# Kernel tuning notes

Hardware: AMD Instinct MI355X
Metric: run time of the kernel (lower is better)

Reference implementation:

```python
import jax, jax.numpy as jnp
from jax import lax
import numpy as np

DIVISOR = 2.0

def setup_inputs() -> dict:
    key = jax.random.key(0)
    k1, k2, k3, k4 = jax.random.split(key, 4)
    B, Cin, D, H, W = 64, 8, 32, 64, 64
    Cout, KD, KH, KW = 16, 3, 3, 3
    fan_in = Cin * KD * KH * KW
    bound = 1.0 / np.sqrt(fan_in)
    x = jax.random.normal(k1, (B, Cin, D, H, W), dtype=jnp.float32)
    conv_weight = jax.random.uniform(k2, (Cout, Cin, KD, KH, KW), jnp.float32, -bound, bound)
    conv_bias = jax.random.uniform(k3, (Cout,), jnp.float32, -bound, bound)
    bias = jax.random.normal(k4, (Cout, 1, 1, 1), dtype=jnp.float32) * 0.02
    return {"x": x, "conv_weight": conv_weight, "conv_bias": conv_bias, "bias": bias}

def reference(x, conv_weight, conv_bias, bias):
    # Conv3d, stride 1, no padding, groups=1  -> [B, Cout, D-2, H-2, W-2]
    y = lax.conv_general_dilated(
        x, conv_weight, window_strides=(1, 1, 1), padding='VALID',
        dimension_numbers=('NCDHW', 'OIDHW', 'NCDHW'))
    y = y + conv_bias[None, :, None, None, None]
    # Divide by constant
    y = y / DIVISOR
    # MaxPool3d(kernel=2, stride=2), floor mode (VALID drops the trailing odd row)
    y = lax.reduce_window(y, -jnp.inf, lax.max,
                          window_dimensions=(1, 1, 2, 2, 2),
                          window_strides=(1, 1, 2, 2, 2), padding='VALID')
    # AdaptiveAvgPool3d((1,1,1)) == global mean over spatial dims
    y = jnp.mean(y, axis=(2, 3, 4), keepdims=True)  # [B, Cout, 1, 1, 1]
    # Bias add (broadcast over batch)
    y = y + bias[None]
    # Sum over channel dim (sum_dim=1, no keepdim)
    return jnp.sum(y, axis=1)  # [B, 1, 1, 1]
```

## Files before the change

### kernel.cpp

```cpp
#include <hip/hip_runtime.h>

typedef __attribute__((ext_vector_type(8))) short short8;
typedef __attribute__((ext_vector_type(4))) float f32x4;
typedef unsigned int u32;

#define ROW_B 1056
#define SLOT_B 10560
#define NSLOT 4
#define CSTRIDE 131072

__device__ __forceinline__ unsigned short f2bf(float f) {
  unsigned u = __builtin_bit_cast(unsigned, f);
  u += 0x7FFFu + ((u >> 16) & 1u);
  return (unsigned short)(u >> 16);
}
__device__ __forceinline__ u32 cvtpk(float lo, float hi) {
  u32 r;
  asm("v_cvt_pk_bf16_f32 %0, %1, %2" : "=v"(r) : "v"(lo), "v"(hi));
  return r;
}

#define LBAR()                                                                \
  {                                                                           \
    asm volatile("s_waitcnt lgkmcnt(0)" ::: "memory");                        \
    __builtin_amdgcn_s_barrier();                                             \
    __builtin_amdgcn_sched_barrier(0);                                        \
  }

#define MFMA1(A, B, C) __builtin_amdgcn_mfma_f32_16x16x32_bf16(A, B, C, 0, 0, 0)

#define RDF(SB, WT, R) (*(const short8*)(smem + (SB) + (R) * ROW_B + physoff[WT]))

#define MGRP(F0, F1, F2, F3, WT, AN, AM, AO, K0, K1, K2)                      \
  {                                                                           \
    if (K0) {                                                                 \
      AN[0][WT] = MFMA1(F0, bfragB[0][0], zf4);                               \
      AN[1][WT] = MFMA1(F1, bfragB[0][0], zf4);                               \
      AN[0][WT] = MFMA1(F1, bfragB[0][1], AN[0][WT]);                         \
      AN[1][WT] = MFMA1(F2, bfragB[0][1], AN[1][WT]);                         \
      AN[0][WT] = MFMA1(F2, bfragB[0][2], AN[0][WT]);                         \
      AN[1][WT] = MFMA1(F3, bfragB[0][2], AN[1][WT]);                         \
    }                                                                         \
    if (K1) {                                                                 \
      AM[0][WT] = MFMA1(F0, bfragB[1][0], AM[0][WT]);                         \
      AM[1][WT] = MFMA1(F1, bfragB[1][0], AM[1][WT]);                         \
      AM[0][WT] = MFMA1(F1, bfragB[1][1], AM[0][WT]);                         \
      AM[1][WT] = MFMA1(F2, bfragB[1][1], AM[1][WT]);                         \
      AM[0][WT] = MFMA1(F2, bfragB[1][2], AM[0][WT]);                         \
      AM[1][WT] = MFMA1(F3, bfragB[1][2], AM[1][WT]);                         \
    }                                                                         \
    if (K2) {                                                                 \
      AO[0][WT] = MFMA1(F0, bfragB[2][0], AO[0][WT]);                         \
      AO[1][WT] = MFMA1(F1, bfragB[2][0], AO[1][WT]);                         \
      AO[0][WT] = MFMA1(F1, bfragB[2][1], AO[0][WT]);                         \
      AO[1][WT] = MFMA1(F2, bfragB[2][1], AO[1][WT]);                         \
      AO[0][WT] = MFMA1(F2, bfragB[2][2], AO[0][WT]);                         \
      AO[1][WT] = MFMA1(F3, bfragB[2][2], AO[1][WT]);                         \
    }                                                                         \
  }

#define PROC(DP, AN, AM, AO, PFC, PFN, K0, K1, K2, CL, SV, WR, LD, PF, BAR)   \
  {                                                                           \
    const int dp_  = (DP);                                                    \
    const int sb_  = (dp_ & 3) * SLOT_B + rowbase;                            \
    const int sbn_ = ((dp_ + 1) & 3) * SLOT_B + rowbase;                      \
    short8 t1_0 = RDF(sb_, 1, 0), t1_1 = RDF(sb_, 1, 1),                      \
           t1_2 = RDF(sb_, 1, 2), t1_3 = RDF(sb_, 1, 3);                      \
    __builtin_amdgcn_s_setprio(1);                                            \
    MGRP(PFC[0], PFC[1], PFC[2], PFC[3], 0, AN, AM, AO, K0, K1, K2);          \
    short8 t2_0 = RDF(sb_, 2, 0), t2_1 = RDF(sb_, 2, 1),                      \
           t2_2 = RDF(sb_, 2, 2), t2_3 = RDF(sb_, 2, 3);                      \
    MGRP(t1_0, t1_1, t1_2, t1_3, 1, AN, AM, AO, K0, K1, K2);                  \
    short8 t3_0 = RDF(sb_, 3, 0), t3_1 = RDF(sb_, 3, 1),                      \
           t3_2 = RDF(sb_, 3, 2), t3_3 = RDF(sb_, 3, 3);                      \
    MGRP(t2_0, t2_1, t2_2, t2_3, 2, AN, AM, AO, K0, K1, K2);                  \
    if (PF) {                                                                 \
      PFN[0] = RDF(sbn_, 0, 0); PFN[1] = RDF(sbn_, 0, 1);                     \
      PFN[2] = RDF(sbn_, 0, 2); PFN[3] = RDF(sbn_, 0, 3);                     \
    }                                                                         \
    MGRP(t3_0, t3_1, t3_2, t3_3, 3, AN, AM, AO, K0, K1, K2);                  \
    __builtin_amdgcn_s_setprio(0);                                            \
    if (WR) stage_write(dp_ + 3);                                             \
    if (LD) stage_load(dp_ + 4);                                              \
    if (CL) {                                                                 \
      _Pragma("unroll") for (int wt = 0; wt < 4; ++wt) {                      \
        const float e01 = fmaxf(fmaxf(AO[0][wt][0], AO[0][wt][1]),            \
                                fmaxf(AO[1][wt][0], AO[1][wt][1]));           \
        const float e23 = fmaxf(fmaxf(AO[0][wt][2], AO[0][wt][3]),            \
                                fmaxf(AO[1][wt][2], AO[1][wt][3]));           \
        if (SV) {                                                             \
          p01[wt] = e01; p23[wt] = e23;                                       \
        } else if (hvalid) {                                                  \
          sum += fmaxf(p01[wt], e01);                                         \
          if (!(wt == 3 && g == 3)) sum += fmaxf(p23[wt], e23);               \
        }                                                                     \
      }                                                                       \
    }                                                                         \
    if (BAR) LBAR()                                                           \
  }

__launch_bounds__(256, 2)
__global__ void conv_fused(const float* __restrict__ x,
                           const float* __restrict__ cw,
                           float* __restrict__ ws) {
  __shared__ __align__(16) unsigned char smem[NSLOT * SLOT_B];
  __shared__ float wsum[4];

  const int rb  = blockIdx.x;
  const int bid = (rb & 7) * 64 + (rb >> 3);
  const int b   = bid >> 3;
  const int hq  = bid & 7;
  const int h0  = hq * 8;

  const int tid  = threadIdx.x;
  const int lane = tid & 63;
  const int wid  = tid >> 6;
  const int nm   = lane & 15;
  const int g    = lane >> 4;

  const float* xb = x + (size_t)b * (8u * 32u * 64u * 64u);

  short8 bfragB[3][3];
#pragma unroll
  for (int kd = 0; kd < 3; ++kd)
#pragma unroll
    for (int kh = 0; kh < 3; ++kh) {
      short8 f;
#pragma unroll
      for (int j = 0; j < 8; ++j) {
        float v = (g < 3) ? cw[(nm * 8 + j) * 27 + kd * 9 + kh * 3 + g] : 0.f;
        f[j] = (short)f2bf(v);
      }
      bfragB[kd][kh] = f;
    }

  const int gc = (g < 3) ? g : 2;
  int physoff[4];
#pragma unroll
  for (int wt = 0; wt < 4; ++wt) physoff[wt] = (wt * 16 + nm + gc) * 16;
  const int rowbase = (2 * wid) * ROW_B;

  bool st_act[3]; int st_toff[3]; int st_off[3];
#pragma unroll
  for (int pass = 0; pass < 3; ++pass) {
    const int t = tid + pass * 256;
    bool act = (t < 640);
    int row = (t >> 6) % 10;
    const int w = t & 63;
    int h = h0 + row;
    if (h > 63) { act = false; h = 63; }
    st_act[pass]  = act;
    st_toff[pass] = h * 64 + w;
    st_off[pass]  = row * ROW_B + w * 16;
  }

  float ld[3][8];

  auto stage_load = [&](int p) {
    const int pbase = p * 4096;
#pragma unroll
    for (int pass = 0; pass < 3; ++pass) {
      if (st_act[pass]) {
        const int o = st_toff[pass] + pbase;
#pragma unroll
        for (int c = 0; c < 8; ++c)
          ld[pass][c] = (xb + (size_t)c * CSTRIDE)[o];
      }
    }
  };
  auto stage_write = [&](int p) {
    unsigned char* d = smem + (p & 3) * SLOT_B;
#pragma unroll
    for (int pass = 0; pass < 3; ++pass) {
      if (st_act[pass]) {
        uint4 v;
        v.x = cvtpk(ld[pass][0], ld[pass][1]);
        v.y = cvtpk(ld[pass][2], ld[pass][3]);
        v.z = cvtpk(ld[pass][4], ld[pass][5]);
        v.w = cvtpk(ld[pass][6], ld[pass][7]);
        *(uint4*)(d + st_off[pass]) = v;
      }
    }
  };

  const bool hvalid = !(hq == 7 && wid == 3);
  const f32x4 zf4 = {0.f, 0.f, 0.f, 0.f};
  float sum = 0.f;
  float p01[4], p23[4];
  f32x4 accA[2][4], accB[2][4], accC[2][4];
  short8 pfA[4], pfB[4];

  stage_load(0); stage_write(0);
  stage_load(1); stage_write(1);
  stage_load(2); stage_write(2);
  stage_load(3);
  LBAR()
  {
    const int pb_ = 0 * SLOT_B + rowbase;
    pfA[0] = RDF(pb_, 0, 0); pfA[1] = RDF(pb_, 0, 1);
    pfA[2] = RDF(pb_, 0, 2); pfA[3] = RDF(pb_, 0, 3);
  }

  PROC(0, accA, accB, accC, pfA, pfB, 1, 0, 0, 0, 0, 1, 1, 1, 1)
  PROC(1, accB, accA, accC, pfB, pfA, 1, 1, 0, 0, 0, 1, 1, 1, 1)

  for (int p0 = 2; p0 <= 20; p0 += 6) {
    PROC(p0 + 0, accC, accB, accA, pfA, pfB, 1, 1, 1, 1, 1, 1, 1, 1, 1)
    PROC(p0 + 1, accA, accC, accB, pfB, pfA, 1, 1, 1, 1, 0, 1, 1, 1, 1)
    PROC(p0 + 2, accB, accA, accC, pfA, pfB, 1, 1, 1, 1, 1, 1, 1, 1, 1)
    PROC(p0 + 3, accC, accB, accA, pfB, pfA, 1, 1, 1, 1, 0, 1, 1, 1, 1)
    PROC(p0 + 4, accA, accC, accB, pfA, pfB, 1, 1, 1, 1, 1, 1, 1, 1, 1)
    PROC(p0 + 5, accB, accA, accC, pfB, pfA, 1, 1, 1, 1, 0, 1, 1, 1, 1)
  }
  PROC(26, accC, accB, accA, pfA, pfB, 1, 1, 1, 1, 1, 1, 1, 1, 1)
  PROC(27, accA, accC, accB, pfB, pfA, 1, 1, 1, 1, 0, 1, 1, 1, 1)
  PROC(28, accB, accA, accC, pfA, pfB, 1, 1, 1, 1, 1, 1, 0, 1, 1)
  PROC(29, accC, accB, accA, pfB, pfA, 1, 1, 1, 1, 0, 0, 0, 1, 1)
  PROC(30, accA, accC, accB, pfA, pfB, 0, 1, 1, 1, 1, 0, 0, 1, 1)
  PROC(31, accB, accA, accC, pfB, pfA, 0, 0, 1, 1, 0, 0, 0, 0, 0)

#pragma unroll
  for (int off = 32; off > 0; off >>= 1) sum += __shfl_down(sum, off);
  if (lane == 0) wsum[wid] = sum;
  __syncthreads();
  if (tid == 0) ws[bid] = wsum[0] + wsum[1] + wsum[2] + wsum[3];
}

__global__ void finalize_k(const float* __restrict__ ws,
                           const float* __restrict__ cb,
                           const float* __restrict__ bias,
                           float* __restrict__ out) {
  const int b = threadIdx.x;
  float s = 0.f;
#pragma unroll
  for (int hq = 0; hq < 8; ++hq) s += ws[b * 8 + hq];
  float cbs = 0.f, bs = 0.f;
#pragma unroll
  for (int c = 0; c < 16; ++c) { cbs += cb[c]; bs += bias[c]; }
  out[b] = 0.5f * s / 14415.f + 0.5f * cbs + bs;
}

extern "C" void kernel_launch(void* const* d_in, const int* in_sizes, int n_in,
                              void* d_out, int out_size, void* d_ws, size_t ws_size,
                              hipStream_t stream) {
  const float* x    = (const float*)d_in[0];
  const float* cw   = (const float*)d_in[1];
  const float* cb   = (const float*)d_in[2];
  const float* bias = (const float*)d_in[3];
  float* out = (float*)d_out;
  float* ws  = (float*)d_ws;

  hipLaunchKernelGGL(conv_fused, dim3(512), dim3(256), 0, stream, x, cw, ws);
  hipLaunchKernelGGL(finalize_k, dim3(1), dim3(64), 0, stream, ws, cb, bias, out);
}
```

Baseline: 90.70 us.

## Split conv into single-wave blocks per output row pair, removing barriers

Restructures the fused conv kernel from 256-thread blocks covering 8 output rows to 64-thread single-wave blocks covering one pooled row pair (31 per batch), giving 1984 blocks. Each wave stages only its own 4 input rows in LDS, so all workgroup barriers and the register prefetch of fragments are removed, and the load pipeline depth drops from 4 to 2 depth planes. Input rows are now re-fetched by neighbouring blocks (4 rows read per 2 output rows, versus 10 per 8 before), which raises global/L2 traffic. The finalize kernel sums 31 partials per batch.

```diff
diff --git a/kernel.cpp b/kernel.cpp
--- a/kernel.cpp
+++ b/kernel.cpp
@@ -4,8 +4,7 @@
 typedef __attribute__((ext_vector_type(4))) float f32x4;
 typedef unsigned int u32;
 
-#define ROW_B 1056
-#define SLOT_B 10560
+#define SLOT_B 4096
 #define NSLOT 4
 #define CSTRIDE 131072
 
@@ -20,16 +19,7 @@
   return r;
 }
 
-#define LBAR()                                                                \
-  {                                                                           \
-    asm volatile("s_waitcnt lgkmcnt(0)" ::: "memory");                        \
-    __builtin_amdgcn_s_barrier();                                             \
-    __builtin_amdgcn_sched_barrier(0);                                        \
-  }
-
 #define MFMA1(A, B, C) __builtin_amdgcn_mfma_f32_16x16x32_bf16(A, B, C, 0, 0, 0)
-
-#define RDF(SB, WT, R) (*(const short8*)(smem + (SB) + (R) * ROW_B + physoff[WT]))
 
 #define MGRP(F0, F1, F2, F3, WT, AN, AM, AO, K0, K1, K2)                      \
   {                                                                           \
@@ -59,29 +49,25 @@
     }                                                                         \
   }
 
-#define PROC(DP, AN, AM, AO, PFC, PFN, K0, K1, K2, CL, SV, WR, LD, PF, BAR)   \
+#define PROC(DP, AN, AM, AO, K0, K1, K2, CL, SV, ST)                          \
   {                                                                           \
-    const int dp_  = (DP);                                                    \
-    const int sb_  = (dp_ & 3) * SLOT_B + rowbase;                            \
-    const int sbn_ = ((dp_ + 1) & 3) * SLOT_B + rowbase;                      \
-    short8 t1_0 = RDF(sb_, 1, 0), t1_1 = RDF(sb_, 1, 1),                      \
-           t1_2 = RDF(sb_, 1, 2), t1_3 = RDF(sb_, 1, 3);                      \
+    const int dp_ = (DP);                                                     \
+    if (ST) {                                                                 \
+      stage_load(dp_ + 2);                                                    \
+      __builtin_amdgcn_sched_barrier(0);                                      \
+    }                                                                         \
+    const int sb_ = (dp_ & 3) * SLOT_B;                                       \
     __builtin_amdgcn_s_setprio(1);                                            \
-    MGRP(PFC[0], PFC[1], PFC[2], PFC[3], 0, AN, AM, AO, K0, K1, K2);          \
-    short8 t2_0 = RDF(sb_, 2, 0), t2_1 = RDF(sb_, 2, 1),                      \
-           t2_2 = RDF(sb_, 2, 2), t2_3 = RDF(sb_, 2, 3);                      \
-    MGRP(t1_0, t1_1, t1_2, t1_3, 1, AN, AM, AO, K0, K1, K2);                  \
-    short8 t3_0 = RDF(sb_, 3, 0), t3_1 = RDF(sb_, 3, 1),                      \
-           t3_2 = RDF(sb_, 3, 2), t3_3 = RDF(sb_, 3, 3);                      \
-    MGRP(t2_0, t2_1, t2_2, t2_3, 2, AN, AM, AO, K0, K1, K2);                  \
-    if (PF) {                                                                 \
-      PFN[0] = RDF(sbn_, 0, 0); PFN[1] = RDF(sbn_, 0, 1);                     \
-      PFN[2] = RDF(sbn_, 0, 2); PFN[3] = RDF(sbn_, 0, 3);                     \
-    }                                                                         \
-    MGRP(t3_0, t3_1, t3_2, t3_3, 3, AN, AM, AO, K0, K1, K2);                  \
+    _Pragma("unroll") for (int wt = 0; wt < 4; ++wt) {                        \
+      const short8 f0 = *(const short8*)(smem + sb_ + 0 * 1024 + physoff[wt]); \
+      const short8 f1 = *(const short8*)(smem + sb_ + 1 * 1024 + physoff[wt]); \
+      const short8 f2 = *(const short8*)(smem + sb_ + 2 * 1024 + physoff[wt]); \
+      const short8 f3 = *(const short8*)(smem + sb_ + 3 * 1024 + physoff[wt]); \
+      MGRP(f0, f1, f2, f3, wt, AN, AM, AO, K0, K1, K2);                       \
+    }                                                                         \
     __builtin_amdgcn_s_setprio(0);                                            \
-    if (WR) stage_write(dp_ + 3);                                             \
-    if (LD) stage_load(dp_ + 4);                                              \
+    __builtin_amdgcn_sched_barrier(0);                                        \
+    if (ST) stage_write(dp_ + 2);                                             \
     if (CL) {                                                                 \
       _Pragma("unroll") for (int wt = 0; wt < 4; ++wt) {                      \
         const float e01 = fmaxf(fmaxf(AO[0][wt][0], AO[0][wt][1]),            \
@@ -90,31 +76,27 @@
                                 fmaxf(AO[1][wt][2], AO[1][wt][3]));           \
         if (SV) {                                                             \
           p01[wt] = e01; p23[wt] = e23;                                       \
-        } else if (hvalid) {                                                  \
+        } else {                                                              \
           sum += fmaxf(p01[wt], e01);                                         \
           if (!(wt == 3 && g == 3)) sum += fmaxf(p23[wt], e23);               \
         }                                                                     \
       }                                                                       \
     }                                                                         \
-    if (BAR) LBAR()                                                           \
   }
 
-__launch_bounds__(256, 2)
+__launch_bounds__(64, 2)
 __global__ void conv_fused(const float* __restrict__ x,
                            const float* __restrict__ cw,
                            float* __restrict__ ws) {
-  __shared__ __align__(16) unsigned char smem[NSLOT * SLOT_B];
-  __shared__ float wsum[4];
+  __shared__ __align__(16) unsigned char smem[NSLOT * SLOT_B + 32];
 
   const int rb  = blockIdx.x;
-  const int bid = (rb & 7) * 64 + (rb >> 3);
-  const int b   = bid >> 3;
-  const int hq  = bid & 7;
-  const int h0  = hq * 8;
-
-  const int tid  = threadIdx.x;
-  const int lane = tid & 63;
-  const int wid  = tid >> 6;
+  const int bid = (rb & 7) * 248 + (rb >> 3);
+  const int b   = bid / 31;
+  const int q   = bid - 31 * b;
+  const int h0  = 2 * q;
+
+  const int lane = threadIdx.x;
   const int nm   = lane & 15;
   const int g    = lane >> 4;
 
@@ -138,92 +120,65 @@
   int physoff[4];
 #pragma unroll
   for (int wt = 0; wt < 4; ++wt) physoff[wt] = (wt * 16 + nm + gc) * 16;
-  const int rowbase = (2 * wid) * ROW_B;
-
-  bool st_act[3]; int st_toff[3]; int st_off[3];
-#pragma unroll
-  for (int pass = 0; pass < 3; ++pass) {
-    const int t = tid + pass * 256;
-    bool act = (t < 640);
-    int row = (t >> 6) % 10;
-    const int w = t & 63;
-    int h = h0 + row;
-    if (h > 63) { act = false; h = 63; }
-    st_act[pass]  = act;
-    st_toff[pass] = h * 64 + w;
-    st_off[pass]  = row * ROW_B + w * 16;
-  }
-
-  float ld[3][8];
+
+  int o_base[4];
+#pragma unroll
+  for (int s = 0; s < 4; ++s) o_base[s] = (h0 + s) * 64 + lane;
+
+  float ld[4][8];
 
   auto stage_load = [&](int p) {
     const int pbase = p * 4096;
 #pragma unroll
-    for (int pass = 0; pass < 3; ++pass) {
-      if (st_act[pass]) {
-        const int o = st_toff[pass] + pbase;
-#pragma unroll
-        for (int c = 0; c < 8; ++c)
-          ld[pass][c] = (xb + (size_t)c * CSTRIDE)[o];
-      }
+    for (int s = 0; s < 4; ++s) {
+      const int o = o_base[s] + pbase;
+#pragma unroll
+      for (int c = 0; c < 8; ++c)
+        ld[s][c] = (xb + (size_t)c * CSTRIDE)[o];
     }
   };
   auto stage_write = [&](int p) {
-    unsigned char* d = smem + (p & 3) * SLOT_B;
-#pragma unroll
-    for (int pass = 0; pass < 3; ++pass) {
-      if (st_act[pass]) {
-        uint4 v;
-        v.x = cvtpk(ld[pass][0], ld[pass][1]);
-        v.y = cvtpk(ld[pass][2], ld[pass][3]);
-        v.z = cvtpk(ld[pass][4], ld[pass][5]);
-        v.w = cvtpk(ld[pass][6], ld[pass][7]);
-        *(uint4*)(d + st_off[pass]) = v;
-      }
+    unsigned char* d = smem + (p & 3) * SLOT_B + lane * 16;
+#pragma unroll
+    for (int s = 0; s < 4; ++s) {
+      uint4 v;
+      v.x = cvtpk(ld[s][0], ld[s][1]);
+      v.y = cvtpk(ld[s][2], ld[s][3]);
+      v.z = cvtpk(ld[s][4], ld[s][5]);
+      v.w = cvtpk(ld[s][6], ld[s][7]);
+      *(uint4*)(d + s * 1024) = v;
     }
   };
 
-  const bool hvalid = !(hq == 7 && wid == 3);
   const f32x4 zf4 = {0.f, 0.f, 0.f, 0.f};
   float sum = 0.f;
   float p01[4], p23[4];
   f32x4 accA[2][4], accB[2][4], accC[2][4];
-  short8 pfA[4], pfB[4];
 
   stage_load(0); stage_write(0);
   stage_load(1); stage_write(1);
-  stage_load(2); stage_write(2);
-  stage_load(3);
-  LBAR()
-  {
-    const int pb_ = 0 * SLOT_B + rowbase;
-    pfA[0] = RDF(pb_, 0, 0); pfA[1] = RDF(pb_, 0, 1);
-    pfA[2] = RDF(pb_, 0, 2); pfA[3] = RDF(pb_, 0, 3);
+
+  PROC(0, accA, accB, accC, 1, 0, 0, 0, 0, 1)
+  PROC(1, accB, accA, accC, 1, 1, 0, 0, 0, 1)
+
+  for (int p0 = 2; p0 <= 20; p0 += 6) {
+    PROC(p0 + 0, accC, accB, accA, 1, 1, 1, 1, 1, 1)
+    PROC(p0 + 1, accA, accC, accB, 1, 1, 1, 1, 0, 1)
+    PROC(p0 + 2, accB, accA, accC, 1, 1, 1, 1, 1, 1)
+    PROC(p0 + 3, accC, accB, accA, 1, 1, 1, 1, 0, 1)
+    PROC(p0 + 4, accA, accC, accB, 1, 1, 1, 1, 1, 1)
+    PROC(p0 + 5, accB, accA, accC, 1, 1, 1, 1, 0, 1)
   }
-
-  PROC(0, accA, accB, accC, pfA, pfB, 1, 0, 0, 0, 0, 1, 1, 1, 1)
-  PROC(1, accB, accA, accC, pfB, pfA, 1, 1, 0, 0, 0, 1, 1, 1, 1)
-
-  for (int p0 = 2; p0 <= 20; p0 += 6) {
-    PROC(p0 + 0, accC, accB, accA, pfA, pfB, 1, 1, 1, 1, 1, 1, 1, 1, 1)
-    PROC(p0 + 1, accA, accC, accB, pfB, pfA, 1, 1, 1, 1, 0, 1, 1, 1, 1)
-    PROC(p0 + 2, accB, accA, accC, pfA, pfB, 1, 1, 1, 1, 1, 1, 1, 1, 1)
-    PROC(p0 + 3, accC, accB, accA, pfB, pfA, 1, 1, 1, 1, 0, 1, 1, 1, 1)
-    PROC(p0 + 4, accA, accC, accB, pfA, pfB, 1, 1, 1, 1, 1, 1, 1, 1, 1)
-    PROC(p0 + 5, accB, accA, accC, pfB, pfA, 1, 1, 1, 1, 0, 1, 1, 1, 1)
-  }
-  PROC(26, accC, accB, accA, pfA, pfB, 1, 1, 1, 1, 1, 1, 1, 1, 1)
-  PROC(27, accA, accC, accB, pfB, pfA, 1, 1, 1, 1, 0, 1, 1, 1, 1)
-  PROC(28, accB, accA, accC, pfA, pfB, 1, 1, 1, 1, 1, 1, 0, 1, 1)
-  PROC(29, accC, accB, accA, pfB, pfA, 1, 1, 1, 1, 0, 0, 0, 1, 1)
-  PROC(30, accA, accC, accB, pfA, pfB, 0, 1, 1, 1, 1, 0, 0, 1, 1)
-  PROC(31, accB, accA, accC, pfB, pfA, 0, 0, 1, 1, 0, 0, 0, 0, 0)
+  PROC(26, accC, accB, accA, 1, 1, 1, 1, 1, 1)
+  PROC(27, accA, accC, accB, 1, 1, 1, 1, 0, 1)
+  PROC(28, accB, accA, accC, 1, 1, 1, 1, 1, 1)
+  PROC(29, accC, accB, accA, 1, 1, 1, 1, 0, 1)
+  PROC(30, accA, accC, accB, 0, 1, 1, 1, 1, 0)
+  PROC(31, accB, accA, accC, 0, 0, 1, 1, 0, 0)
 
 #pragma unroll
   for (int off = 32; off > 0; off >>= 1) sum += __shfl_down(sum, off);
-  if (lane == 0) wsum[wid] = sum;
-  __syncthreads();
-  if (tid == 0) ws[bid] = wsum[0] + wsum[1] + wsum[2] + wsum[3];
+  if (lane == 0) ws[bid] = sum;
 }
 
 __global__ void finalize_k(const float* __restrict__ ws,
@@ -233,7 +188,7 @@
   const int b = threadIdx.x;
   float s = 0.f;
 #pragma unroll
-  for (int hq = 0; hq < 8; ++hq) s += ws[b * 8 + hq];
+  for (int q = 0; q < 31; ++q) s += ws[b * 31 + q];
   float cbs = 0.f, bs = 0.f;
 #pragma unroll
   for (int c = 0; c < 16; ++c) { cbs += cb[c]; bs += bias[c]; }
@@ -250,6 +205,6 @@
   float* out = (float*)d_out;
   float* ws  = (float*)d_ws;
 
-  hipLaunchKernelGGL(conv_fused, dim3(512), dim3(256), 0, stream, x, cw, ws);
+  hipLaunchKernelGGL(conv_fused, dim3(1984), dim3(64), 0, stream, x, cw, ws);
   hipLaunchKernelGGL(finalize_k, dim3(1), dim3(64), 0, stream, ws, cb, bias, out);
 }
```

Result: faster. 78.80 us (-13.1%).
